# Kernel tuning notes

Hardware: AMD Instinct MI355X
Metric: run time of the kernel (lower is better)

Reference implementation:

```python
import jax, jax.numpy as jnp
import numpy as np

B, T, F, H = 4096, 512, 32, 32  # batch, seq_len, input_size, hidden_size


def setup_inputs() -> dict:
    key = jax.random.key(0)
    ks = jax.random.split(key, 7)
    s = 1.0 / np.sqrt(H)  # torch LSTM/Linear init scale
    return {
        "x": jax.random.normal(ks[0], (B, T, F), dtype=jnp.float32),
        "W_ih": jax.random.uniform(ks[1], (4 * H, F), minval=-s, maxval=s, dtype=jnp.float32),
        "W_hh": jax.random.uniform(ks[2], (4 * H, H), minval=-s, maxval=s, dtype=jnp.float32),
        "b_ih": jax.random.uniform(ks[3], (4 * H,), minval=-s, maxval=s, dtype=jnp.float32),
        "b_hh": jax.random.uniform(ks[4], (4 * H,), minval=-s, maxval=s, dtype=jnp.float32),
        "W_fc": jax.random.uniform(ks[5], (1, H), minval=-s, maxval=s, dtype=jnp.float32),
        "b_fc": jax.random.uniform(ks[6], (1,), minval=-s, maxval=s, dtype=jnp.float32),
    }


def _lstm_last_hidden(x, W_ih, W_hh, b_ih, b_hh):
    # Precompute input-to-gate projections for all timesteps in one GEMM.
    # Gate packing order (PyTorch): i, f, g, o.
    h_dim = W_hh.shape[1]
    xg = jnp.einsum("btf,gf->btg", x, W_ih) + (b_ih + b_hh)  # [B,T,4H]
    xg = jnp.transpose(xg, (1, 0, 2))  # [T,B,4H] for scan over time

    def step(carry, g_x):
        h, c = carry
        gates = g_x + h @ W_hh.T  # [B,4H]
        i = jax.nn.sigmoid(gates[:, 0 * h_dim:1 * h_dim])
        f = jax.nn.sigmoid(gates[:, 1 * h_dim:2 * h_dim])
        g = jnp.tanh(gates[:, 2 * h_dim:3 * h_dim])
        o = jax.nn.sigmoid(gates[:, 3 * h_dim:4 * h_dim])
        c_new = f * c + i * g
        h_new = o * jnp.tanh(c_new)
        return (h_new, c_new), None

    h0 = jnp.zeros((x.shape[0], h_dim), dtype=x.dtype)
    c0 = jnp.zeros_like(h0)
    (h_last, _), _ = jax.lax.scan(step, (h0, c0), xg)
    return h_last  # [B,H]


def reference(x, W_ih, W_hh, b_ih, b_hh, W_fc, b_fc):
    h_last = _lstm_last_hidden(x, W_ih, W_hh, b_ih, b_hh)
    # Dropout is identity in eval mode (reference baseline is deterministic).
    logits = h_last @ W_fc.T + b_fc  # [B,1]
    return jnp.squeeze(logits, -1)  # [B]
```

## Files before the change

### kernel.cpp

```cpp
#include <hip/hip_runtime.h>
#include <stdint.h>


typedef _Float16 half8 __attribute__((ext_vector_type(8)));
typedef __attribute__((ext_vector_type(4))) float float4v;

#define T_LEN 512
#define B_ALL 4096
#define ROWS 16
#define NBLK (B_ALL / ROWS)
#define P 40

__global__ __launch_bounds__(512, 2) void lstm_fused_kernel(
    const float* __restrict__ x,
    const float* __restrict__ W_ih,
    const float* __restrict__ W_hh,
    const float* __restrict__ b_ih,
    const float* __restrict__ b_hh,
    const float* __restrict__ W_fc,
    const float* __restrict__ b_fc,
    float* __restrict__ out)
{
    const int tid  = threadIdx.x;
    const int wv   = tid >> 6;
    const int lane = tid & 63;
    const int col  = lane & 15;
    const int q    = lane >> 4;
    const int k0   = q * 8;
    const int b0   = blockIdx.x * ROWS;
    const int e    = 4 * wv + q;

    __shared__ __align__(16) _Float16 hs[2][ROWS][P];
    __shared__ __align__(16) _Float16 xs[4][ROWS][P];

    half8 wih, whh;
    {
        const int gt   = col & 3;
        const int gmem = gt * 32 + (4 * wv + (col >> 2));
        const float gs = (gt == 2) ? 2.88539008f : -1.44269504f;
        const float* wr = W_ih + gmem * 32 + k0;
        const float* hr = W_hh + gmem * 32 + k0;
        #pragma unroll
        for (int i = 0; i < 8; ++i) {
            wih[i] = (_Float16)(wr[i] * gs);
            whh[i] = (_Float16)(hr[i] * gs);
        }
    }
    float4v bias4;
    #pragma unroll
    for (int r = 0; r < 4; ++r) {
        const float gsr = (r == 2) ? 2.88539008f : -1.44269504f;
        bias4[r] = (b_ih[r * 32 + e] + b_hh[r * 32 + e]) * gsr;
    }

    float c = 0.f;

    const int sr = tid >> 5;
    const int sk = tid & 31;
    const float* xsrc = x + ((size_t)(b0 + sr) * T_LEN) * 32 + sk;

    float xA, xB;
    {
        xs[0][sr][sk] = (_Float16)xsrc[0];
        xs[1][sr][sk] = (_Float16)xsrc[32];
        xs[2][sr][sk] = (_Float16)xsrc[64];
        hs[0][sr][sk] = (_Float16)0.f;
        xA = xsrc[3 * 32];
        xB = xsrc[4 * 32];
    }
    __syncthreads();

    float4v a1c;
    {
        const half8 ax0 = *(const half8*)&xs[0][col][k0];
        a1c = __builtin_amdgcn_mfma_f32_16x16x32_f16(wih, ax0, bias4, 0, 0, 0);
    }

    #define STEP(PPAR, XREG, TT)                                                \
    {                                                                           \
        const int xq = ((TT) + 1) & 3;                                          \
        const int xw = ((TT) + 3) & 3;                                          \
        const half8 ah  = *(const half8*)&hs[PPAR][col][k0];      \
        const half8 axn = *(const half8*)&xs[xq][col][k0];     \
                           \
        const float4v acc =                                                     \
            __builtin_amdgcn_mfma_f32_16x16x32_f16(whh, ah, a1c, 0, 0, 0);      \
                                \
        a1c = __builtin_amdgcn_mfma_f32_16x16x32_f16(wih, axn, bias4, 0, 0, 0); \
        {                   \
            xs[xw][sr][sk] = (_Float16)XREG;                                    \
            int tn = (TT) + 5; if (tn >= T_LEN) tn = T_LEN - 1;                 \
            XREG = xsrc[(size_t)tn * 32];                                       \
        }                                                                       \
         \
          \
        const float Ai = __builtin_amdgcn_exp2f(acc[0]);                        \
        const float Af = __builtin_amdgcn_exp2f(acc[1]);                        \
        const float Bg = __builtin_amdgcn_exp2f(acc[2]);                        \
        const float Ao = __builtin_amdgcn_exp2f(acc[3]);                        \
        const float pI = 1.0f + Ai;                                             \
        const float pG = 1.0f + Bg;                                             \
        const float pF = 1.0f + Af;                                             \
        const float pIG = pI * pG;                                              \
        const float num = c * pIG + (Bg - 1.0f) * pF;                           \
        c = num * __builtin_amdgcn_rcpf(pF * pIG);                              \
        const float cc = fminf(fmaxf(c, -16.0f), 16.0f);                        \
        const float C2 = __builtin_amdgcn_exp2f(cc * 2.88539008f);              \
        const float r3 = __builtin_amdgcn_rcpf((1.0f + Ao) * (1.0f + C2));      \
        const float hv = (C2 - 1.0f) * r3;                                      \
        hs[PPAR ^ 1][col][e] = (_Float16)hv;                                    \
        __syncthreads();                                                        \
    }

    for (int t = 0; t < T_LEN; t += 2) {
        STEP(0, xA, t)
        STEP(1, xB, t + 1)
    }
    #undef STEP

    if (tid < ROWS) {
        float s = b_fc[0];
        #pragma unroll
        for (int cc2 = 0; cc2 < 32; ++cc2) {
            s += (float)hs[0][tid][cc2] * W_fc[cc2];
        }
        out[b0 + tid] = s;
    }
}

extern "C" void kernel_launch(void* const* d_in, const int* in_sizes, int n_in,
                              void* d_out, int out_size, void* d_ws, size_t ws_size,
                              hipStream_t stream) {
    const float* x    = (const float*)d_in[0];
    const float* W_ih = (const float*)d_in[1];
    const float* W_hh = (const float*)d_in[2];
    const float* b_ih = (const float*)d_in[3];
    const float* b_hh = (const float*)d_in[4];
    const float* W_fc = (const float*)d_in[5];
    const float* b_fc = (const float*)d_in[6];
    float* out = (float*)d_out;

    lstm_fused_kernel<<<dim3(NBLK), dim3(512), 0, stream>>>(
        x, W_ih, W_hh, b_ih, b_hh, W_fc, b_fc, out);
}
```

Measured before the change: 137.2 us.

## Load x directly into MFMA operand registers, dropping the shared-memory x staging

Each lane now reads its own eight x values straight from global memory as two float4 loads and converts them to fp16 in registers, keeping a three-step register prefetch ring. The shared-memory x ring buffer and its per-step store are removed, cutting LDS traffic and the shared read in each recurrent step. In exchange, each wave issues redundant global loads, since the four waves all load the same x rows, and register pressure rises from the six extra float4 prefetch registers.

New measurement: 243.1 us. +77.3%, slower.

```diff
diff --git a/kernel.cpp b/kernel.cpp
--- a/kernel.cpp
+++ b/kernel.cpp
@@ -31,7 +31,6 @@
     const int e    = 4 * wv + q;
 
     __shared__ __align__(16) _Float16 hs[2][ROWS][P];
-    __shared__ __align__(16) _Float16 xs[4][ROWS][P];
 
     half8 wih, whh;
     {
@@ -55,42 +54,46 @@
 
     float c = 0.f;
 
-    const int sr = tid >> 5;
-    const int sk = tid & 31;
-    const float* xsrc = x + ((size_t)(b0 + sr) * T_LEN) * 32 + sk;
-
-    float xA, xB;
-    {
-        xs[0][sr][sk] = (_Float16)xsrc[0];
-        xs[1][sr][sk] = (_Float16)xsrc[32];
-        xs[2][sr][sk] = (_Float16)xsrc[64];
-        hs[0][sr][sk] = (_Float16)0.f;
-        xA = xsrc[3 * 32];
-        xB = xsrc[4 * 32];
-    }
-    __syncthreads();
+    const float* xrow = x + (size_t)(b0 + col) * (T_LEN * 32) + k0;
 
     float4v a1c;
     {
-        const half8 ax0 = *(const half8*)&xs[0][col][k0];
+        float4v v0 = *(const float4v*)(xrow);
+        float4v v1 = *(const float4v*)(xrow + 4);
+        half8 ax0;
+        ax0[0] = (_Float16)v0[0]; ax0[1] = (_Float16)v0[1];
+        ax0[2] = (_Float16)v0[2]; ax0[3] = (_Float16)v0[3];
+        ax0[4] = (_Float16)v1[0]; ax0[5] = (_Float16)v1[1];
+        ax0[6] = (_Float16)v1[2]; ax0[7] = (_Float16)v1[3];
         a1c = __builtin_amdgcn_mfma_f32_16x16x32_f16(wih, ax0, bias4, 0, 0, 0);
     }
+    float4v xa0 = *(const float4v*)(xrow + 1 * 32);
+    float4v xa1 = *(const float4v*)(xrow + 1 * 32 + 4);
+    float4v xb0 = *(const float4v*)(xrow + 2 * 32);
+    float4v xb1 = *(const float4v*)(xrow + 2 * 32 + 4);
+    float4v xc0 = *(const float4v*)(xrow + 3 * 32);
+    float4v xc1 = *(const float4v*)(xrow + 3 * 32 + 4);
 
-    #define STEP(PPAR, XREG, TT)                                                \
+    hs[0][tid >> 5][tid & 31] = (_Float16)0.f;
+    __syncthreads();
+
+    #define STEP(PPAR, TT)                                                      \
     {                                                                           \
-        const int xq = ((TT) + 1) & 3;                                          \
-        const int xw = ((TT) + 3) & 3;                                          \
-        const half8 ah  = *(const half8*)&hs[PPAR][col][k0];      \
-        const half8 axn = *(const half8*)&xs[xq][col][k0];     \
-                           \
+        const half8 ah = *(const half8*)&hs[PPAR][col][k0];       \
         const float4v acc =                                                     \
             __builtin_amdgcn_mfma_f32_16x16x32_f16(whh, ah, a1c, 0, 0, 0);      \
                                 \
+        half8 axn;                                                              \
+        axn[0] = (_Float16)xa0[0]; axn[1] = (_Float16)xa0[1];                   \
+        axn[2] = (_Float16)xa0[2]; axn[3] = (_Float16)xa0[3];                   \
+        axn[4] = (_Float16)xa1[0]; axn[5] = (_Float16)xa1[1];                   \
+        axn[6] = (_Float16)xa1[2]; axn[7] = (_Float16)xa1[3];                   \
         a1c = __builtin_amdgcn_mfma_f32_16x16x32_f16(wih, axn, bias4, 0, 0, 0); \
-        {                   \
-            xs[xw][sr][sk] = (_Float16)XREG;                                    \
-            int tn = (TT) + 5; if (tn >= T_LEN) tn = T_LEN - 1;                 \
-            XREG = xsrc[(size_t)tn * 32];                                       \
+        xa0 = xb0; xa1 = xb1; xb0 = xc0; xb1 = xc1;                             \
+        {                                                                       \
+            int tn = (TT) + 4; if (tn >= T_LEN) tn = T_LEN - 1;                 \
+            xc0 = *(const float4v*)(xrow + (size_t)tn * 32);                    \
+            xc1 = *(const float4v*)(xrow + (size_t)tn * 32 + 4);                \
         }                                                                       \
          \
           \
@@ -113,8 +116,8 @@
     }
 
     for (int t = 0; t < T_LEN; t += 2) {
-        STEP(0, xA, t)
-        STEP(1, xB, t + 1)
+        STEP(0, t)
+        STEP(1, t + 1)
     }
     #undef STEP
 
```

## Halve block to four waves, each computing two gate tiles per step

Applied to the files above, without the earlier changes.

Each block now runs 256 threads instead of 512. Every wave holds two sets of W_ih/W_hh fragments and issues two MFMAs per projection, covering two hidden-unit groups (e0 and e0+16). The x staging loads now fetch float2 pairs per thread. The aim is to cut per-step barrier cost and wave count per block, and to give more independent work per wave to hide MFMA and transcendental latency. In exchange it raises register pressure and puts more serial per-wave work on the recurrent critical path, and the launch bounds change from 2 to 1 minimum blocks.

New measurement: 144.9 us. 5.7% more time.

```diff
diff --git a/kernel.cpp b/kernel.cpp
--- a/kernel.cpp
+++ b/kernel.cpp
@@ -3,7 +3,9 @@
 
 
 typedef _Float16 half8 __attribute__((ext_vector_type(8)));
+typedef _Float16 half2v __attribute__((ext_vector_type(2)));
 typedef __attribute__((ext_vector_type(4))) float float4v;
+typedef __attribute__((ext_vector_type(2))) float float2v;
 
 #define T_LEN 512
 #define B_ALL 4096
@@ -11,7 +13,7 @@
 #define NBLK (B_ALL / ROWS)
 #define P 40
 
-__global__ __launch_bounds__(512, 2) void lstm_fused_kernel(
+__global__ __launch_bounds__(256, 1) void lstm_fused_kernel(
     const float* __restrict__ x,
     const float* __restrict__ W_ih,
     const float* __restrict__ W_hh,
@@ -28,87 +30,121 @@
     const int q    = lane >> 4;
     const int k0   = q * 8;
     const int b0   = blockIdx.x * ROWS;
-    const int e    = 4 * wv + q;
+    const int e0   = 4 * wv + q;
+    const int e1   = e0 + 16;
 
     __shared__ __align__(16) _Float16 hs[2][ROWS][P];
     __shared__ __align__(16) _Float16 xs[4][ROWS][P];
 
-    half8 wih, whh;
+    half8 wih0, whh0, wih1, whh1;
+    float4v bias0, bias1;
     {
-        const int gt   = col & 3;
-        const int gmem = gt * 32 + (4 * wv + (col >> 2));
+        const int gt = col & 3;
         const float gs = (gt == 2) ? 2.88539008f : -1.44269504f;
-        const float* wr = W_ih + gmem * 32 + k0;
-        const float* hr = W_hh + gmem * 32 + k0;
+        const int g0 = gt * 32 + (4 * wv + (col >> 2));
+        const int g1 = gt * 32 + (4 * (wv + 4) + (col >> 2));
+        const float* wr0 = W_ih + g0 * 32 + k0;
+        const float* hr0 = W_hh + g0 * 32 + k0;
+        const float* wr1 = W_ih + g1 * 32 + k0;
+        const float* hr1 = W_hh + g1 * 32 + k0;
         #pragma unroll
         for (int i = 0; i < 8; ++i) {
-            wih[i] = (_Float16)(wr[i] * gs);
-            whh[i] = (_Float16)(hr[i] * gs);
+            wih0[i] = (_Float16)(wr0[i] * gs);
+            whh0[i] = (_Float16)(hr0[i] * gs);
+            wih1[i] = (_Float16)(wr1[i] * gs);
+            whh1[i] = (_Float16)(hr1[i] * gs);
+        }
+        #pragma unroll
+        for (int r = 0; r < 4; ++r) {
+            const float gsr = (r == 2) ? 2.88539008f : -1.44269504f;
+            bias0[r] = (b_ih[r * 32 + e0] + b_hh[r * 32 + e0]) * gsr;
+            bias1[r] = (b_ih[r * 32 + e1] + b_hh[r * 32 + e1]) * gsr;
         }
     }
-    float4v bias4;
-    #pragma unroll
-    for (int r = 0; r < 4; ++r) {
-        const float gsr = (r == 2) ? 2.88539008f : -1.44269504f;
-        bias4[r] = (b_ih[r * 32 + e] + b_hh[r * 32 + e]) * gsr;
-    }
 
-    float c = 0.f;
+    float c0 = 0.f, c1 = 0.f;
 
-    const int sr = tid >> 5;
-    const int sk = tid & 31;
-    const float* xsrc = x + ((size_t)(b0 + sr) * T_LEN) * 32 + sk;
+    const int sr = tid >> 4;
+    const int k2 = (tid & 15) << 1;
+    const float* xsrc = x + ((size_t)(b0 + sr) * T_LEN) * 32 + k2;
 
-    float xA, xB;
+    float2v xA, xB;
     {
-        xs[0][sr][sk] = (_Float16)xsrc[0];
-        xs[1][sr][sk] = (_Float16)xsrc[32];
-        xs[2][sr][sk] = (_Float16)xsrc[64];
-        hs[0][sr][sk] = (_Float16)0.f;
-        xA = xsrc[3 * 32];
-        xB = xsrc[4 * 32];
+        float2v v0 = *(const float2v*)(xsrc);
+        float2v v1 = *(const float2v*)(xsrc + 32);
+        float2v v2 = *(const float2v*)(xsrc + 64);
+        half2v h0; h0[0] = (_Float16)v0[0]; h0[1] = (_Float16)v0[1];
+        half2v h1; h1[0] = (_Float16)v1[0]; h1[1] = (_Float16)v1[1];
+        half2v h2; h2[0] = (_Float16)v2[0]; h2[1] = (_Float16)v2[1];
+        *(half2v*)&xs[0][sr][k2] = h0;
+        *(half2v*)&xs[1][sr][k2] = h1;
+        *(half2v*)&xs[2][sr][k2] = h2;
+        half2v hz; hz[0] = (_Float16)0.f; hz[1] = (_Float16)0.f;
+        *(half2v*)&hs[0][sr][k2] = hz;
+        xA = *(const float2v*)(xsrc + 3 * 32);
+        xB = *(const float2v*)(xsrc + 4 * 32);
     }
     __syncthreads();
 
-    float4v a1c;
+    float4v a1c0, a1c1;
     {
         const half8 ax0 = *(const half8*)&xs[0][col][k0];
-        a1c = __builtin_amdgcn_mfma_f32_16x16x32_f16(wih, ax0, bias4, 0, 0, 0);
+        a1c0 = __builtin_amdgcn_mfma_f32_16x16x32_f16(wih0, ax0, bias0, 0, 0, 0);
+        a1c1 = __builtin_amdgcn_mfma_f32_16x16x32_f16(wih1, ax0, bias1, 0, 0, 0);
     }
 
     #define STEP(PPAR, XREG, TT)                                                \
     {                                                                           \
-        const int xq = ((TT) + 1) & 3;                                          \
-        const int xw = ((TT) + 3) & 3;                                          \
-        const half8 ah  = *(const half8*)&hs[PPAR][col][k0];      \
-        const half8 axn = *(const half8*)&xs[xq][col][k0];     \
-                           \
-        const float4v acc =                                                     \
-            __builtin_amdgcn_mfma_f32_16x16x32_f16(whh, ah, a1c, 0, 0, 0);      \
-                                \
-        a1c = __builtin_amdgcn_mfma_f32_16x16x32_f16(wih, axn, bias4, 0, 0, 0); \
-        {                   \
-            xs[xw][sr][sk] = (_Float16)XREG;                                    \
+        const half8 ah = *(const half8*)&hs[PPAR][col][k0];       \
+        const float4v acc0 =                                                    \
+            __builtin_amdgcn_mfma_f32_16x16x32_f16(whh0, ah, a1c0, 0, 0, 0);    \
+        const float4v acc1 =                                                    \
+            __builtin_amdgcn_mfma_f32_16x16x32_f16(whh1, ah, a1c1, 0, 0, 0);    \
+              \
+        const half8 axn = *(const half8*)&xs[((TT) + 1) & 3][col][k0];          \
+        a1c0 = __builtin_amdgcn_mfma_f32_16x16x32_f16(wih0, axn, bias0, 0,0,0); \
+        a1c1 = __builtin_amdgcn_mfma_f32_16x16x32_f16(wih1, axn, bias1, 0,0,0); \
+        {                  \
+            half2v hx;                                                          \
+            hx[0] = (_Float16)XREG[0]; hx[1] = (_Float16)XREG[1];               \
+            *(half2v*)&xs[((TT) + 3) & 3][sr][k2] = hx;                         \
             int tn = (TT) + 5; if (tn >= T_LEN) tn = T_LEN - 1;                 \
-            XREG = xsrc[(size_t)tn * 32];                                       \
+            XREG = *(const float2v*)(xsrc + (size_t)tn * 32);                   \
         }                                                                       \
-         \
-          \
-        const float Ai = __builtin_amdgcn_exp2f(acc[0]);                        \
-        const float Af = __builtin_amdgcn_exp2f(acc[1]);                        \
-        const float Bg = __builtin_amdgcn_exp2f(acc[2]);                        \
-        const float Ao = __builtin_amdgcn_exp2f(acc[3]);                        \
-        const float pI = 1.0f + Ai;                                             \
-        const float pG = 1.0f + Bg;                                             \
-        const float pF = 1.0f + Af;                                             \
-        const float pIG = pI * pG;                                              \
-        const float num = c * pIG + (Bg - 1.0f) * pF;                           \
-        c = num * __builtin_amdgcn_rcpf(pF * pIG);                              \
-        const float cc = fminf(fmaxf(c, -16.0f), 16.0f);                        \
-        const float C2 = __builtin_amdgcn_exp2f(cc * 2.88539008f);              \
-        const float r3 = __builtin_amdgcn_rcpf((1.0f + Ao) * (1.0f + C2));      \
-        const float hv = (C2 - 1.0f) * r3;                                      \
-        hs[PPAR ^ 1][col][e] = (_Float16)hv;                                    \
+                            \
+        {                                                                       \
+            const float Ai = __builtin_amdgcn_exp2f(acc0[0]);                   \
+            const float Af = __builtin_amdgcn_exp2f(acc0[1]);                   \
+            const float Bg = __builtin_amdgcn_exp2f(acc0[2]);                   \
+            const float Ao = __builtin_amdgcn_exp2f(acc0[3]);                   \
+            const float pI = 1.0f + Ai;                                         \
+            const float pG = 1.0f + Bg;                                         \
+            const float pF = 1.0f + Af;                                         \
+            const float pIG = pI * pG;                                          \
+            const float num = c0 * pIG + (Bg - 1.0f) * pF;                      \
+            c0 = num * __builtin_amdgcn_rcpf(pF * pIG);                         \
+            const float cc = fminf(fmaxf(c0, -16.0f), 16.0f);                   \
+            const float C2 = __builtin_amdgcn_exp2f(cc * 2.88539008f);          \
+            const float r3 = __builtin_amdgcn_rcpf((1.0f + Ao) * (1.0f + C2));  \
+            hs[PPAR ^ 1][col][e0] = (_Float16)((C2 - 1.0f) * r3);               \
+        }                                                                       \
+                                                       \
+        {                                                                       \
+            const float Ai = __builtin_amdgcn_exp2f(acc1[0]);                   \
+            const float Af = __builtin_amdgcn_exp2f(acc1[1]);                   \
+            const float Bg = __builtin_amdgcn_exp2f(acc1[2]);                   \
+            const float Ao = __builtin_amdgcn_exp2f(acc1[3]);                   \
+            const float pI = 1.0f + Ai;                                         \
+            const float pG = 1.0f + Bg;                                         \
+            const float pF = 1.0f + Af;                                         \
+            const float pIG = pI * pG;                                          \
+            const float num = c1 * pIG + (Bg - 1.0f) * pF;                      \
+            c1 = num * __builtin_amdgcn_rcpf(pF * pIG);                         \
+            const float cc = fminf(fmaxf(c1, -16.0f), 16.0f);                   \
+            const float C2 = __builtin_amdgcn_exp2f(cc * 2.88539008f);          \
+            const float r3 = __builtin_amdgcn_rcpf((1.0f + Ao) * (1.0f + C2));  \
+            hs[PPAR ^ 1][col][e1] = (_Float16)((C2 - 1.0f) * r3);               \
+        }                                                                       \
         __syncthreads();                                                        \
     }
 
@@ -140,6 +176,6 @@
     const float* b_fc = (const float*)d_in[6];
     float* out = (float*)d_out;
 
-    lstm_fused_kernel<<<dim3(NBLK), dim3(512), 0, stream>>>(
+    lstm_fused_kernel<<<dim3(NBLK), dim3(256), 0, stream>>>(
         x, W_ih, W_hh, b_ih, b_hh, W_fc, b_fc, out);
 }
```
